# Kernel tuning notes

Hardware: AMD Instinct MI355X
Metric: run time of the kernel (lower is better)

The kernel has to match this reference:

```python
import jax, jax.numpy as jnp
import numpy as np

B, C, H, W = 4, 128, 64, 64
CO = 128

def setup_inputs() -> dict:
    key = jax.random.key(0)
    ks = jax.random.split(key, 10)
    s = 1.0 / np.sqrt(C)
    return {
        "x":  jax.random.normal(ks[0], (B, C, H, W), dtype=jnp.float32),
        "Wq": jax.random.uniform(ks[1], (C, C), jnp.float32, -s, s),
        "bq": jax.random.uniform(ks[2], (C,), jnp.float32, -s, s),
        "Wk": jax.random.uniform(ks[3], (C, C), jnp.float32, -s, s),
        "bk": jax.random.uniform(ks[4], (C,), jnp.float32, -s, s),
        "Wv": jax.random.uniform(ks[5], (C, C), jnp.float32, -s, s),
        "bv": jax.random.uniform(ks[6], (C,), jnp.float32, -s, s),
        "gamma": jnp.ones((1,), dtype=jnp.float32),
        "Wo": jax.random.uniform(ks[7], (CO, C), jnp.float32, -s, s),
        "bo": jax.random.uniform(ks[8], (CO,), jnp.float32, -s, s),
    }

def reference(x, Wq, bq, Wk, bk, Wv, bv, gamma, Wo, bo):
    b, c, h, w = x.shape
    xf = x.reshape(b, c, h * w)                       # [B,C,N]
    # 1x1 convs == channel matmuls
    Q = jnp.einsum('oc,bcn->bon', Wq, xf) + bq[None, :, None]
    K = jnp.einsum('oc,bcn->bon', Wk, xf) + bk[None, :, None]
    V = jnp.einsum('oc,bcn->bon', Wv, xf) + bv[None, :, None]
    # attention[b,i,j] = softmax_j( sum_c Q[b,c,i] K[b,c,j] )  (unscaled)
    scores = jnp.einsum('bci,bcj->bij', Q, K)         # [B,N,N]
    attn = jax.nn.softmax(scores, axis=-1)
    # selfAtten[b,c,i] = sum_j V[b,c,j] attn[b,i,j]
    sa = jnp.einsum('bcj,bij->bci', V, attn)          # [B,C,N]
    sa = gamma[0] * sa + xf
    out = jnp.einsum('oc,bcn->bon', Wo, sa) + bo[None, :, None]
    return out.reshape(b, Wo.shape[0], h, w)
```

## Files before the change

kernel.cpp:

```cpp
#include <hip/hip_runtime.h>

#define BB 4
#define CC 128
#define NN 4096

typedef float f32x4 __attribute__((ext_vector_type(4)));
typedef __bf16 bf16x8 __attribute__((ext_vector_type(8)));

#define MFMA16(A, B, C) __builtin_amdgcn_mfma_f32_16x16x32_bf16((A), (B), (C), 0, 0, 0)

typedef __attribute__((address_space(3))) void lds_void;
typedef __attribute__((address_space(1))) void glob_void;
#define GLD16(g, l) __builtin_amdgcn_global_load_lds((const glob_void*)(g), (lds_void*)(l), 16, 0, 0)

__device__ __forceinline__ int fK(int r) { return (r & 3) | (((r >> 3) & 1) << 2); }

__global__ __launch_bounds__(256)
void pack_w(const float* __restrict__ Wq, const float* __restrict__ bq,
            const float* __restrict__ Wk, const float* __restrict__ bk,
            const float* __restrict__ Wv, const float* __restrict__ bv,
            const float* __restrict__ Wo, const float* __restrict__ bo,
            __bf16* __restrict__ Wpk, float* __restrict__ bpk)
{
    const int mat = blockIdx.x >> 3;
    const int p   = blockIdx.x & 7;
    const int tid = threadIdx.x;
    const int ks  = tid >> 6;
    const int lane = tid & 63;
    const int col = lane & 15;
    const int quad = lane >> 4;

    const float LOG2E = 1.44269504088896340736f;
    const float* W = (mat == 0) ? Wq : (mat == 1) ? Wk : (mat == 2) ? Wv : Wo;
    const float* bsrc = (mat == 0) ? bq : (mat == 1) ? bk : (mat == 2) ? bv : bo;
    const float scale = (mat == 0) ? LOG2E : 1.0f;

    const float* wr = W + (size_t)(p * 16 + col) * CC + ks * 32 + quad * 8;
    float4 f0 = *(const float4*)wr;
    float4 f1 = *(const float4*)(wr + 4);
    bf16x8 a;
    a[0]=(__bf16)(f0.x*scale); a[1]=(__bf16)(f0.y*scale);
    a[2]=(__bf16)(f0.z*scale); a[3]=(__bf16)(f0.w*scale);
    a[4]=(__bf16)(f1.x*scale); a[5]=(__bf16)(f1.y*scale);
    a[6]=(__bf16)(f1.z*scale); a[7]=(__bf16)(f1.w*scale);
    *(bf16x8*)&Wpk[(((size_t)(mat * 8 + p) * 4 + ks) * 64 + lane) * 8] = a;

    if (p == 0 && tid < 128) bpk[mat * 128 + tid] = bsrc[tid] * scale;
}

__global__ __launch_bounds__(256, 2)
void qkv_gemm(const float* __restrict__ x,
              const __bf16* __restrict__ Wpk, const float* __restrict__ bpk,
              __bf16* __restrict__ Qt, __bf16* __restrict__ Kt,
              __bf16* __restrict__ Vblk)
{
    const int b    = blockIdx.y;
    const int n0   = blockIdx.x * 32;
    const int tid  = threadIdx.x;
    const int lane = tid & 63;
    const int wv   = __builtin_amdgcn_readfirstlane(tid >> 6);
    const int col  = lane & 15;
    const int quad = lane >> 4;

    __shared__ __bf16 xs[32 * 144];
    __shared__ __bf16 vs[128 * 32];

    {
        const int n  = tid & 31;
        const int c0 = tid >> 5;
        const float* xb = x + ((size_t)b * CC) * NN + n0 + n;
#pragma unroll
        for (int i = 0; i < 8; i++) {
            int c = (c0 + i * 8) * 2;
            float v0 = xb[(size_t)c * NN];
            float v1 = xb[(size_t)(c + 1) * NN];
            union { __bf16 h[2]; unsigned u; } pk;
            pk.h[0] = (__bf16)v0; pk.h[1] = (__bf16)v1;
            *(unsigned*)&xs[n * 144 + c] = pk.u;
        }
    }
    __syncthreads();

    bf16x8 Bf[2][4];
#pragma unroll
    for (int ng = 0; ng < 2; ng++)
#pragma unroll
        for (int ks = 0; ks < 4; ks++)
            Bf[ng][ks] = *(const bf16x8*)&xs[(ng * 16 + col) * 144 + ks * 32 + quad * 8];

#pragma unroll 1
    for (int p = 0; p < 6; p++) {
        const int mat = p >> 1;
        const int pg  = wv + 4 * (p & 1);
        const int o0  = pg * 16;

        bf16x8 Af[4];
#pragma unroll
        for (int ks = 0; ks < 4; ks++)
            Af[ks] = *(const bf16x8*)&Wpk[(((size_t)(mat * 8 + pg) * 4 + ks) * 64 + lane) * 8];

        f32x4 D[2];
#pragma unroll
        for (int ng = 0; ng < 2; ng++) D[ng] = (f32x4){0.f, 0.f, 0.f, 0.f};
#pragma unroll
        for (int ks = 0; ks < 4; ks++)
#pragma unroll
            for (int ng = 0; ng < 2; ng++)
                D[ng] = MFMA16(Af[ks], Bf[ng][ks], D[ng]);

        float4 bias = *(const float4*)(bpk + mat * 128 + o0 + quad * 4);

#pragma unroll
        for (int ng = 0; ng < 2; ng++) {
            const int n = ng * 16 + col;
            float v[4];
#pragma unroll
            for (int r = 0; r < 4; r++)
                v[r] = D[ng][r] + ((const float*)&bias)[r];
            if (mat == 0) {
                union { __bf16 h[4]; uint2 u; } pk;
                for (int r = 0; r < 4; r++) pk.h[r] = (__bf16)v[r];
                *(uint2*)&Qt[((size_t)b * NN + n0 + n) * CC + o0 + quad * 4] = pk.u;
            } else if (mat == 1) {
                const int rin = ((n0 & 32) + n) & 63;
                const int chunk = ((o0 + quad * 4) >> 3) ^ fK(rin);
                union { __bf16 h[4]; uint2 u; } pk;
                for (int r = 0; r < 4; r++) pk.h[r] = (__bf16)v[r];
                *(uint2*)&Kt[((size_t)b * NN + n0 + n) * CC + chunk * 8 + (quad & 1) * 4] = pk.u;
            } else {
#pragma unroll
                for (int r = 0; r < 4; r++)
                    vs[(o0 + quad * 4 + r) * 32 + n] = (__bf16)v[r];
            }
        }
    }
    __syncthreads();

    {
        __bf16* vd = Vblk + (((size_t)b * 64 + (n0 >> 6)) * CC) * 64;
        const int chbase = (n0 & 32) >> 3;
#pragma unroll
        for (int e = 0; e < 2; e++) {
            int idx = e * 256 + tid;
            int c = idx >> 2, chl = idx & 3;
            bf16x8 v = *(const bf16x8*)&vs[c * 32 + chl * 8];
            *(bf16x8*)&vd[c * 64 + (((chbase + chl) ^ (c & 7)) * 8)] = v;
        }
    }
}

__global__ __launch_bounds__(256, 3)
void flash_attn(const __bf16* __restrict__ Qt, const __bf16* __restrict__ Kt,
                const __bf16* __restrict__ Vblk,
                float* __restrict__ Opart, float* __restrict__ Lpart)
{
    const int blk = blockIdx.x;
    const int b    = blk & 3;
    const int jlow = (blk >> 2) & 1;
    const int jhigh = (blk >> 3) & 3;
    const int it32  = blk >> 5;
    const int js   = (jhigh << 1) | jlow;
    const int i0   = it32 * 128;

    const int tid  = threadIdx.x;
    const int lane = tid & 63;
    const int iw   = __builtin_amdgcn_readfirstlane(tid >> 6);
    const int col  = lane & 15;
    const int quad = lane >> 4;

    __shared__ __align__(16) char smem[34816];
    char* Kbytes = smem;
    char* Vbytes = smem + 16384;
    __bf16* Vh = (__bf16*)Vbytes;

#pragma unroll
    for (int e = 0; e < 4; e++) {
        int k = e * 256 + tid;
        Vh[128 * 64 + k] = (__bf16)((k < 64) ? 1.0f : 0.0f);
    }

    const __bf16* Qb = Qt + (size_t)b * NN * CC;
    const char*   Ks = (const char*)(Kt + (size_t)b * NN * CC);
    const char*   Vs = (const char*)(Vblk + ((size_t)b * 64 * CC) * 64);

    const int ibase = i0 + iw * 32;

    bf16x8 qf[2][4];
#pragma unroll
    for (int ig = 0; ig < 2; ig++)
#pragma unroll
        for (int ks = 0; ks < 4; ks++)
            qf[ig][ks] = *(const bf16x8*)(Qb + (size_t)(ibase + ig * 16 + col) * CC
                                             + ks * 32 + quad * 8);

    const int perm = ((col & 12) << 1) | (col & 3);
    const int fR   = fK(perm);
    int kaddr[4][4];
    const int joff[4] = {0, 4, 32, 36};
#pragma unroll
    for (int jg = 0; jg < 4; jg++)
#pragma unroll
        for (int ks = 0; ks < 4; ks++)
            kaddr[jg][ks] = (perm + joff[jg]) * 256 + (((ks * 4 + quad) ^ fR) * 16);
    int vaddr[8][2], oaddr[2];
#pragma unroll
    for (int cg = 0; cg < 8; cg++)
#pragma unroll
        for (int t = 0; t < 2; t++)
            vaddr[cg][t] = (cg * 16 + col) * 128 + (((t * 4 + quad) ^ (col & 7)) * 16);
#pragma unroll
    for (int t = 0; t < 2; t++)
        oaddr[t] = (128 + col) * 128 + (t * 4 + quad) * 16;

    f32x4 O[2][8], lacc[2];
#pragma unroll
    for (int ig = 0; ig < 2; ig++) {
#pragma unroll
        for (int cg = 0; cg < 8; cg++) O[ig][cg] = (f32x4){0.f, 0.f, 0.f, 0.f};
        lacc[ig] = (f32x4){0.f, 0.f, 0.f, 0.f};
    }

#pragma unroll 1
    for (int t8 = 0; t8 < 8; t8++) {
        const int jt = js * 8 + t8;
        const char* kg = Ks + (size_t)jt * 16384;
        const char* vg = Vs + (size_t)jt * 16384;
#pragma unroll
        for (int q = 0; q < 4; q++) {
            const int call = iw * 4 + q;
            GLD16(kg + call * 1024 + lane * 16, Kbytes + call * 1024 + lane * 16);
            GLD16(vg + call * 1024 + lane * 16, Vbytes + call * 1024 + lane * 16);
        }
        __syncthreads();

        f32x4 S[2][4];
#pragma unroll
        for (int ig = 0; ig < 2; ig++)
#pragma unroll
            for (int jg = 0; jg < 4; jg++)
                S[ig][jg] = (f32x4){-32.f, -32.f, -32.f, -32.f};
#pragma unroll
        for (int ks = 0; ks < 4; ks++) {
            bf16x8 k0 = *(const bf16x8*)(Kbytes + kaddr[0][ks]);
            bf16x8 k1 = *(const bf16x8*)(Kbytes + kaddr[1][ks]);
            bf16x8 k2 = *(const bf16x8*)(Kbytes + kaddr[2][ks]);
            bf16x8 k3 = *(const bf16x8*)(Kbytes + kaddr[3][ks]);
            S[0][0] = MFMA16(k0, qf[0][ks], S[0][0]);
            S[1][0] = MFMA16(k0, qf[1][ks], S[1][0]);
            S[0][1] = MFMA16(k1, qf[0][ks], S[0][1]);
            S[1][1] = MFMA16(k1, qf[1][ks], S[1][1]);
            S[0][2] = MFMA16(k2, qf[0][ks], S[0][2]);
            S[1][2] = MFMA16(k2, qf[1][ks], S[1][2]);
            S[0][3] = MFMA16(k3, qf[0][ks], S[0][3]);
            S[1][3] = MFMA16(k3, qf[1][ks], S[1][3]);
        }

#pragma unroll
        for (int ig = 0; ig < 2; ig++)
#pragma unroll
            for (int jg = 0; jg < 4; jg++)
#pragma unroll
                for (int r = 0; r < 4; r++)
                    S[ig][jg][r] = __builtin_amdgcn_exp2f(S[ig][jg][r]);

#pragma unroll
        for (int t = 0; t < 2; t++) {
            bf16x8 pf0, pf1;
#pragma unroll
            for (int e = 0; e < 8; e++) {
                int jg = 2 * t + (e >> 2), r = e & 3;
                pf0[e] = (__bf16)S[0][jg][r];
                pf1[e] = (__bf16)S[1][jg][r];
            }
#pragma unroll
            for (int cg = 0; cg < 8; cg++) {
                bf16x8 vf = *(const bf16x8*)(Vbytes + vaddr[cg][t]);
                O[0][cg] = MFMA16(vf, pf0, O[0][cg]);
                O[1][cg] = MFMA16(vf, pf1, O[1][cg]);
            }
            bf16x8 of = *(const bf16x8*)(Vbytes + oaddr[t]);
            lacc[0] = MFMA16(of, pf0, lacc[0]);
            lacc[1] = MFMA16(of, pf1, lacc[1]);
        }
        __syncthreads();
    }

    {
        float* Od = Opart + (((size_t)b * 8 + js) * CC) * NN + ibase;
#pragma unroll
        for (int ig = 0; ig < 2; ig++)
#pragma unroll
            for (int cg = 0; cg < 8; cg++)
#pragma unroll
                for (int r = 0; r < 4; r++)
                    Od[(size_t)(cg * 16 + quad * 4 + r) * NN + ig * 16 + col]
                        = O[ig][cg][r];
        if (quad == 0) {
            float* Ld = Lpart + ((size_t)b * 8 + js) * NN + ibase;
#pragma unroll
            for (int ig = 0; ig < 2; ig++)
                Ld[ig * 16 + col] = lacc[ig][0];
        }
    }
}

__global__ __launch_bounds__(256, 2)
void proj_out(const float* __restrict__ Opart, const float* __restrict__ Lpart,
              const float* __restrict__ x,
              const __bf16* __restrict__ Wpk, const float* __restrict__ bpk,
              const float* __restrict__ gamma, float* __restrict__ out)
{
    const int b    = blockIdx.y;
    const int n0   = blockIdx.x * 32;
    const int tid  = threadIdx.x;
    const int lane = tid & 63;
    const int wv   = __builtin_amdgcn_readfirstlane(tid >> 6);
    const int col  = lane & 15;
    const int quad = lane >> 4;

    __shared__ __bf16 sas[32 * 144];
    __shared__ float  outs[128 * 34];

    const float g = gamma[0];

    {
        const int n  = tid & 31;
        const int c0 = tid >> 5;
        const size_t nb = (size_t)b * 8;
        float l = 0.f;
#pragma unroll
        for (int jsp = 0; jsp < 8; jsp++)
            l += Lpart[(nb + jsp) * NN + n0 + n];
        const float gl = g / l;
        const float* xb = x + ((size_t)b * CC) * NN + n0 + n;
        const float* Ob = Opart + (nb * CC) * NN + n0 + n;
#pragma unroll
        for (int i = 0; i < 8; i++) {
            int c = (c0 + i * 8) * 2;
            float s0 = 0.f, s1 = 0.f;
#pragma unroll
            for (int jsp = 0; jsp < 8; jsp++) {
                s0 += Ob[((size_t)jsp * CC + c) * NN];
                s1 += Ob[((size_t)jsp * CC + c + 1) * NN];
            }
            float v0 = xb[(size_t)c * NN] + s0 * gl;
            float v1 = xb[(size_t)(c + 1) * NN] + s1 * gl;
            union { __bf16 h[2]; unsigned u; } pk;
            pk.h[0] = (__bf16)v0; pk.h[1] = (__bf16)v1;
            *(unsigned*)&sas[n * 144 + c] = pk.u;
        }
    }
    __syncthreads();

    bf16x8 Bf[2][4];
#pragma unroll
    for (int ng = 0; ng < 2; ng++)
#pragma unroll
        for (int ks = 0; ks < 4; ks++)
            Bf[ng][ks] = *(const bf16x8*)&sas[(ng * 16 + col) * 144 + ks * 32 + quad * 8];

#pragma unroll
    for (int p = 0; p < 2; p++) {
        const int pg = wv * 2 + p;
        const int o0 = pg * 16;
        bf16x8 Af[4];
#pragma unroll
        for (int ks = 0; ks < 4; ks++)
            Af[ks] = *(const bf16x8*)&Wpk[(((size_t)(3 * 8 + pg) * 4 + ks) * 64 + lane) * 8];

        f32x4 D[2];
#pragma unroll
        for (int ng = 0; ng < 2; ng++) D[ng] = (f32x4){0.f, 0.f, 0.f, 0.f};
#pragma unroll
        for (int ks = 0; ks < 4; ks++)
#pragma unroll
            for (int ng = 0; ng < 2; ng++)
                D[ng] = MFMA16(Af[ks], Bf[ng][ks], D[ng]);

        float4 bias = *(const float4*)(bpk + 3 * 128 + o0 + quad * 4);
#pragma unroll
        for (int ng = 0; ng < 2; ng++)
#pragma unroll
            for (int r = 0; r < 4; r++)
                outs[(o0 + quad * 4 + r) * 34 + ng * 16 + col]
                    = D[ng][r] + ((const float*)&bias)[r];
    }
    __syncthreads();

    {
        float* od = out + ((size_t)b * CC) * NN + n0;
#pragma unroll
        for (int e = 0; e < 16; e++) {
            int k = e * 256 + tid;
            int o = k >> 5, n = k & 31;
            od[(size_t)o * NN + n] = outs[o * 34 + n];
        }
    }
}

extern "C" void kernel_launch(void* const* d_in, const int* in_sizes, int n_in,
                              void* d_out, int out_size, void* d_ws, size_t ws_size,
                              hipStream_t stream)
{
    const float* x  = (const float*)d_in[0];
    const float* Wq = (const float*)d_in[1];
    const float* bq = (const float*)d_in[2];
    const float* Wk = (const float*)d_in[3];
    const float* bk = (const float*)d_in[4];
    const float* Wv = (const float*)d_in[5];
    const float* bv = (const float*)d_in[6];
    const float* gm = (const float*)d_in[7];
    const float* Wo = (const float*)d_in[8];
    const float* bo = (const float*)d_in[9];

    __bf16* Qt    = (__bf16*)d_ws;
    __bf16* Kt    = Qt + (size_t)BB * NN * CC;
    __bf16* Vblk  = Kt + (size_t)BB * NN * CC;
    float*  Opart = (float*)(Vblk + (size_t)BB * NN * CC);
    float*  Lpart = Opart + (size_t)32 * CC * NN;
    __bf16* Wpk   = (__bf16*)(Lpart + (size_t)32 * NN);
    float*  bpk   = (float*)(Wpk + 4 * 8 * 4 * 64 * 8);
    float*  out   = (float*)d_out;

    pack_w<<<32, 256, 0, stream>>>(Wq, bq, Wk, bk, Wv, bv, Wo, bo, Wpk, bpk);
    qkv_gemm<<<dim3(128, 4), 256, 0, stream>>>(x, Wpk, bpk, Qt, Kt, Vblk);
    flash_attn<<<1024, 256, 0, stream>>>(Qt, Kt, Vblk, Opart, Lpart);
    proj_out<<<dim3(128, 4), 256, 0, stream>>>(Opart, Lpart, x, Wpk, bpk, gm, out);
}
```

Baseline: 145.9 us.

## Double-buffer K/V tiles in flash attention and halve the KV split count

The flash attention kernel now prefetches the next K/V tile into a second LDS buffer while computing on the current one, which removes the load-then-wait stall on each iteration. The KV dimension is split into 4 partitions instead of 8 (512 blocks, 16 tiles each), which halves the partial-output traffic that proj_out must read and reduce. Output partials are staged through LDS so they can be written with coalesced float4 stores. qkv_gemm moves to 512-thread blocks so each wave handles one output group per matrix. The cost is roughly double the LDS per block (about 68 KB) and fewer blocks, which lowers occupancy and parallelism.

```diff
diff --git a/kernel.cpp b/kernel.cpp
--- a/kernel.cpp
+++ b/kernel.cpp
@@ -48,7 +48,7 @@
     if (p == 0 && tid < 128) bpk[mat * 128 + tid] = bsrc[tid] * scale;
 }
 
-__global__ __launch_bounds__(256, 2)
+__global__ __launch_bounds__(512, 2)
 void qkv_gemm(const float* __restrict__ x,
               const __bf16* __restrict__ Wpk, const float* __restrict__ bpk,
               __bf16* __restrict__ Qt, __bf16* __restrict__ Kt,
@@ -70,8 +70,8 @@
         const int c0 = tid >> 5;
         const float* xb = x + ((size_t)b * CC) * NN + n0 + n;
 #pragma unroll
-        for (int i = 0; i < 8; i++) {
-            int c = (c0 + i * 8) * 2;
+        for (int i = 0; i < 4; i++) {
+            int c = (c0 + i * 16) * 2;
             float v0 = xb[(size_t)c * NN];
             float v1 = xb[(size_t)(c + 1) * NN];
             union { __bf16 h[2]; unsigned u; } pk;
@@ -89,10 +89,9 @@
             Bf[ng][ks] = *(const bf16x8*)&xs[(ng * 16 + col) * 144 + ks * 32 + quad * 8];
 
 #pragma unroll 1
-    for (int p = 0; p < 6; p++) {
-        const int mat = p >> 1;
-        const int pg  = wv + 4 * (p & 1);
-        const int o0  = pg * 16;
+    for (int mat = 0; mat < 3; mat++) {
+        const int pg = wv;
+        const int o0 = pg * 16;
 
         bf16x8 Af[4];
 #pragma unroll
@@ -139,28 +138,24 @@
     {
         __bf16* vd = Vblk + (((size_t)b * 64 + (n0 >> 6)) * CC) * 64;
         const int chbase = (n0 & 32) >> 3;
-#pragma unroll
-        for (int e = 0; e < 2; e++) {
-            int idx = e * 256 + tid;
-            int c = idx >> 2, chl = idx & 3;
-            bf16x8 v = *(const bf16x8*)&vs[c * 32 + chl * 8];
-            *(bf16x8*)&vd[c * 64 + (((chbase + chl) ^ (c & 7)) * 8)] = v;
-        }
+        int idx = tid;
+        int c = idx >> 2, chl = idx & 3;
+        bf16x8 v = *(const bf16x8*)&vs[c * 32 + chl * 8];
+        *(bf16x8*)&vd[c * 64 + (((chbase + chl) ^ (c & 7)) * 8)] = v;
     }
 }
 
-__global__ __launch_bounds__(256, 3)
+__global__ __launch_bounds__(256, 2)
 void flash_attn(const __bf16* __restrict__ Qt, const __bf16* __restrict__ Kt,
                 const __bf16* __restrict__ Vblk,
                 float* __restrict__ Opart, float* __restrict__ Lpart)
 {
     const int blk = blockIdx.x;
-    const int b    = blk & 3;
-    const int jlow = (blk >> 2) & 1;
-    const int jhigh = (blk >> 3) & 3;
-    const int it32  = blk >> 5;
-    const int js   = (jhigh << 1) | jlow;
-    const int i0   = it32 * 128;
+    const int b   = blk & 3;
+    const int jhi = (blk >> 2) & 1;
+    const int rr  = blk >> 3;
+    const int js  = jhi * 2 + (rr & 1);
+    const int i0  = (rr >> 1) * 128;
 
     const int tid  = threadIdx.x;
     const int lane = tid & 63;
@@ -168,15 +163,13 @@
     const int col  = lane & 15;
     const int quad = lane >> 4;
 
-    __shared__ __align__(16) char smem[34816];
-    char* Kbytes = smem;
-    char* Vbytes = smem + 16384;
-    __bf16* Vh = (__bf16*)Vbytes;
-
-#pragma unroll
-    for (int e = 0; e < 4; e++) {
+    __shared__ __align__(16) char smem[69632];
+
+#pragma unroll
+    for (int e = 0; e < 8; e++) {
         int k = e * 256 + tid;
-        Vh[128 * 64 + k] = (__bf16)((k < 64) ? 1.0f : 0.0f);
+        __bf16* Vh = (__bf16*)(smem + (k >> 10) * 34816 + 16384);
+        Vh[8192 + (k & 1023)] = (__bf16)(((k & 1023) < 64) ? 1.0f : 0.0f);
     }
 
     const __bf16* Qb = Qt + (size_t)b * NN * CC;
@@ -207,10 +200,10 @@
     for (int cg = 0; cg < 8; cg++)
 #pragma unroll
         for (int t = 0; t < 2; t++)
-            vaddr[cg][t] = (cg * 16 + col) * 128 + (((t * 4 + quad) ^ (col & 7)) * 16);
+            vaddr[cg][t] = 16384 + (cg * 16 + col) * 128 + (((t * 4 + quad) ^ (col & 7)) * 16);
 #pragma unroll
     for (int t = 0; t < 2; t++)
-        oaddr[t] = (128 + col) * 128 + (t * 4 + quad) * 16;
+        oaddr[t] = 16384 + (128 + col) * 128 + (t * 4 + quad) * 16;
 
     f32x4 O[2][8], lacc[2];
 #pragma unroll
@@ -220,18 +213,35 @@
         lacc[ig] = (f32x4){0.f, 0.f, 0.f, 0.f};
     }
 
-#pragma unroll 1
-    for (int t8 = 0; t8 < 8; t8++) {
-        const int jt = js * 8 + t8;
-        const char* kg = Ks + (size_t)jt * 16384;
-        const char* vg = Vs + (size_t)jt * 16384;
+    {
+        const char* kg = Ks + (size_t)(js * 16) * 16384;
+        const char* vg = Vs + (size_t)(js * 16) * 16384;
 #pragma unroll
         for (int q = 0; q < 4; q++) {
             const int call = iw * 4 + q;
-            GLD16(kg + call * 1024 + lane * 16, Kbytes + call * 1024 + lane * 16);
-            GLD16(vg + call * 1024 + lane * 16, Vbytes + call * 1024 + lane * 16);
-        }
+            GLD16(kg + call * 1024 + lane * 16, smem + call * 1024 + lane * 16);
+            GLD16(vg + call * 1024 + lane * 16, smem + 16384 + call * 1024 + lane * 16);
+        }
+    }
+
+#pragma unroll 1
+    for (int t16 = 0; t16 < 16; t16++) {
         __syncthreads();
+
+        char* Buf = smem + (t16 & 1) * 34816;
+
+        if (t16 < 15) {
+            const int jt = js * 16 + t16 + 1;
+            const char* kg = Ks + (size_t)jt * 16384;
+            const char* vg = Vs + (size_t)jt * 16384;
+            char* kd = smem + ((t16 + 1) & 1) * 34816;
+#pragma unroll
+            for (int q = 0; q < 4; q++) {
+                const int call = iw * 4 + q;
+                GLD16(kg + call * 1024 + lane * 16, kd + call * 1024 + lane * 16);
+                GLD16(vg + call * 1024 + lane * 16, kd + 16384 + call * 1024 + lane * 16);
+            }
+        }
 
         f32x4 S[2][4];
 #pragma unroll
@@ -241,10 +251,10 @@
                 S[ig][jg] = (f32x4){-32.f, -32.f, -32.f, -32.f};
 #pragma unroll
         for (int ks = 0; ks < 4; ks++) {
-            bf16x8 k0 = *(const bf16x8*)(Kbytes + kaddr[0][ks]);
-            bf16x8 k1 = *(const bf16x8*)(Kbytes + kaddr[1][ks]);
-            bf16x8 k2 = *(const bf16x8*)(Kbytes + kaddr[2][ks]);
-            bf16x8 k3 = *(const bf16x8*)(Kbytes + kaddr[3][ks]);
+            bf16x8 k0 = *(const bf16x8*)(Buf + kaddr[0][ks]);
+            bf16x8 k1 = *(const bf16x8*)(Buf + kaddr[1][ks]);
+            bf16x8 k2 = *(const bf16x8*)(Buf + kaddr[2][ks]);
+            bf16x8 k3 = *(const bf16x8*)(Buf + kaddr[3][ks]);
             S[0][0] = MFMA16(k0, qf[0][ks], S[0][0]);
             S[1][0] = MFMA16(k0, qf[1][ks], S[1][0]);
             S[0][1] = MFMA16(k1, qf[0][ks], S[0][1]);
@@ -274,33 +284,40 @@
             }
 #pragma unroll
             for (int cg = 0; cg < 8; cg++) {
-                bf16x8 vf = *(const bf16x8*)(Vbytes + vaddr[cg][t]);
+                bf16x8 vf = *(const bf16x8*)(Buf + vaddr[cg][t]);
                 O[0][cg] = MFMA16(vf, pf0, O[0][cg]);
                 O[1][cg] = MFMA16(vf, pf1, O[1][cg]);
             }
-            bf16x8 of = *(const bf16x8*)(Vbytes + oaddr[t]);
+            bf16x8 of = *(const bf16x8*)(Buf + oaddr[t]);
             lacc[0] = MFMA16(of, pf0, lacc[0]);
             lacc[1] = MFMA16(of, pf1, lacc[1]);
         }
-        __syncthreads();
-    }
-
-    {
-        float* Od = Opart + (((size_t)b * 8 + js) * CC) * NN + ibase;
-#pragma unroll
-        for (int ig = 0; ig < 2; ig++)
-#pragma unroll
-            for (int cg = 0; cg < 8; cg++)
-#pragma unroll
-                for (int r = 0; r < 4; r++)
-                    Od[(size_t)(cg * 16 + quad * 4 + r) * NN + ig * 16 + col]
-                        = O[ig][cg][r];
-        if (quad == 0) {
-            float* Ld = Lpart + ((size_t)b * 8 + js) * NN + ibase;
-#pragma unroll
-            for (int ig = 0; ig < 2; ig++)
-                Ld[ig * 16 + col] = lacc[ig][0];
-        }
+    }
+    __syncthreads();
+
+    float* Ol = (float*)smem;
+    float* Ll = (float*)(smem + 67584);
+#pragma unroll
+    for (int ig = 0; ig < 2; ig++) {
+#pragma unroll
+        for (int cg = 0; cg < 8; cg++)
+#pragma unroll
+            for (int r = 0; r < 4; r++)
+                Ol[(cg * 16 + quad * 4 + r) * 132 + iw * 32 + ig * 16 + col] = O[ig][cg][r];
+        if (quad == 0) Ll[iw * 32 + ig * 16 + col] = lacc[ig][0];
+    }
+    __syncthreads();
+    {
+        float* Od = Opart + (((size_t)b * 4 + js) * CC) * NN + i0;
+#pragma unroll
+        for (int e = 0; e < 16; e++) {
+            int k = e * 256 + tid;
+            int c = k >> 5, i4 = (k & 31) * 4;
+            float4 v = *(const float4*)(Ol + c * 132 + i4);
+            *(float4*)(Od + (size_t)c * NN + i4) = v;
+        }
+        if (tid < 128)
+            Lpart[((size_t)b * 4 + js) * NN + i0 + tid] = Ll[tid];
     }
 }
 
@@ -326,11 +343,9 @@
     {
         const int n  = tid & 31;
         const int c0 = tid >> 5;
-        const size_t nb = (size_t)b * 8;
-        float l = 0.f;
-#pragma unroll
-        for (int jsp = 0; jsp < 8; jsp++)
-            l += Lpart[(nb + jsp) * NN + n0 + n];
+        const size_t nb = (size_t)b * 4;
+        float l = Lpart[(nb + 0) * NN + n0 + n] + Lpart[(nb + 1) * NN + n0 + n]
+                + Lpart[(nb + 2) * NN + n0 + n] + Lpart[(nb + 3) * NN + n0 + n];
         const float gl = g / l;
         const float* xb = x + ((size_t)b * CC) * NN + n0 + n;
         const float* Ob = Opart + (nb * CC) * NN + n0 + n;
@@ -339,7 +354,7 @@
             int c = (c0 + i * 8) * 2;
             float s0 = 0.f, s1 = 0.f;
 #pragma unroll
-            for (int jsp = 0; jsp < 8; jsp++) {
+            for (int jsp = 0; jsp < 4; jsp++) {
                 s0 += Ob[((size_t)jsp * CC + c) * NN];
                 s1 += Ob[((size_t)jsp * CC + c + 1) * NN];
             }
@@ -417,13 +432,13 @@
     __bf16* Kt    = Qt + (size_t)BB * NN * CC;
     __bf16* Vblk  = Kt + (size_t)BB * NN * CC;
     float*  Opart = (float*)(Vblk + (size_t)BB * NN * CC);
-    float*  Lpart = Opart + (size_t)32 * CC * NN;
-    __bf16* Wpk   = (__bf16*)(Lpart + (size_t)32 * NN);
+    float*  Lpart = Opart + (size_t)16 * CC * NN;
+    __bf16* Wpk   = (__bf16*)(Lpart + (size_t)16 * NN);
     float*  bpk   = (float*)(Wpk + 4 * 8 * 4 * 64 * 8);
     float*  out   = (float*)d_out;
 
     pack_w<<<32, 256, 0, stream>>>(Wq, bq, Wk, bk, Wv, bv, Wo, bo, Wpk, bpk);
-    qkv_gemm<<<dim3(128, 4), 256, 0, stream>>>(x, Wpk, bpk, Qt, Kt, Vblk);
-    flash_attn<<<1024, 256, 0, stream>>>(Qt, Kt, Vblk, Opart, Lpart);
+    qkv_gemm<<<dim3(128, 4), 512, 0, stream>>>(x, Wpk, bpk, Qt, Kt, Vblk);
+    flash_attn<<<512, 256, 0, stream>>>(Qt, Kt, Vblk, Opart, Lpart);
     proj_out<<<dim3(128, 4), 256, 0, stream>>>(Opart, Lpart, x, Wpk, bpk, gm, out);
 }
```

Result: faster. 130.1 us (-10.8%).
